# Performance work log

Measured on AMD Instinct MI355X. Metric: run time of the kernel, lower is better.

## Reference

```python
import jax, jax.numpy as jnp
import numpy as np

N, D, E = 50000, 128, 800000
NEG_SLOPE = 0.2


def setup_inputs() -> dict:
    key = jax.random.key(0)
    ks = jax.random.split(key, 16)
    src = jax.random.randint(ks[0], (E,), 0, N)
    dst = jax.random.randint(ks[1], (E,), 0, N)
    dst = jnp.where(src == dst, (dst + 1) % N, dst)  # no pre-existing self loops (PyG strips them)
    edge_index = jnp.stack([src, dst]).astype(jnp.int32)
    s = 1.0 / np.sqrt(D)  # glorot-ish scale
    return {
        'edge_index': edge_index,
        'embed': jax.random.normal(ks[2], (N, D), jnp.float32),
        'Wl1': jax.random.normal(ks[3], (D, D), jnp.float32) * s,
        'bl1': jnp.zeros((D,), jnp.float32),
        'Wr1': jax.random.normal(ks[4], (D, D), jnp.float32) * s,
        'br1': jnp.zeros((D,), jnp.float32),
        'att1': jax.random.normal(ks[5], (4, D // 4), jnp.float32) * s,
        'b1': jnp.zeros((D,), jnp.float32),
        'Wl2': jax.random.normal(ks[6], (D, D), jnp.float32) * s,
        'bl2': jnp.zeros((D,), jnp.float32),
        'Wr2': jax.random.normal(ks[7], (D, D), jnp.float32) * s,
        'br2': jnp.zeros((D,), jnp.float32),
        'att2': jax.random.normal(ks[8], (1, D), jnp.float32) * s,
        'b2': jnp.zeros((D,), jnp.float32),
    }


def gatv2(x, src, dst, Wl, bl, Wr, br, att, bias, heads, out_ch):
    n = x.shape[0]
    xl = (x @ Wl + bl).reshape(n, heads, out_ch)  # source-side messages
    xr = (x @ Wr + br).reshape(n, heads, out_ch)  # target-side
    e = jax.nn.leaky_relu(xl[src] + xr[dst], NEG_SLOPE)      # [E, H, C]
    score = jnp.einsum('ehc,hc->eh', e, att)                  # [E, H]
    # segment softmax over incoming edges of each target node
    smax = jax.ops.segment_max(score, dst, num_segments=n)
    ex = jnp.exp(score - smax[dst])
    denom = jax.ops.segment_sum(ex, dst, num_segments=n)
    alpha = ex / (denom[dst] + 1e-16)                         # [E, H]
    out = jax.ops.segment_sum(xl[src] * alpha[:, :, None], dst, num_segments=n)
    return out.reshape(n, heads * out_ch) + bias


def reference(edge_index, embed, Wl1, bl1, Wr1, br1, att1, b1,
              Wl2, bl2, Wr2, br2, att2, b2):
    loops = jnp.arange(N, dtype=edge_index.dtype)
    src = jnp.concatenate([edge_index[0], loops])  # add_self_loops=True (PyG default)
    dst = jnp.concatenate([edge_index[1], loops])
    x = gatv2(embed, src, dst, Wl1, bl1, Wr1, br1, att1, b1, 4, D // 4)
    x = jax.nn.relu(x)
    return gatv2(x, src, dst, Wl2, bl2, Wr2, br2, att2, b2, 1, D)
```

## Files before the change

kernel.cpp:

```cpp
#include <hip/hip_runtime.h>
#include <hip/hip_bf16.h>

#define NEG_SLOPE 0.2f
#define CAP 80
#define BNODES 256
#define BCAP 5120
#define CHUNK 4352

typedef unsigned short u16;
typedef short v8s __attribute__((ext_vector_type(8)));
typedef float v4f __attribute__((ext_vector_type(4)));

__device__ __forceinline__ u16 f32_to_bf16(float f) {
    unsigned u = __float_as_uint(f);
    u += 0x7fffu + ((u >> 16) & 1u);
    return (u16)(u >> 16);
}
__device__ __forceinline__ float4 bf16x4_to_f4(uint2 u) {
    float4 f;
    f.x = __uint_as_float(u.x << 16);
    f.y = __uint_as_float(u.x & 0xffff0000u);
    f.z = __uint_as_float(u.y << 16);
    f.w = __uint_as_float(u.y & 0xffff0000u);
    return f;
}

__global__ __launch_bounds__(256)
void prep(const float* __restrict__ Wa, const float* __restrict__ Wb,
          const float* __restrict__ Wc, const float* __restrict__ Wd,
          u16* __restrict__ dst, int* __restrict__ gcur, int nb)
{
    int g = blockIdx.x * 256 + threadIdx.x;
    if (g < nb) gcur[g] = 0;
    if (g >= 8192) return;
    int mat = g >> 11, rem = g & 2047;
    int f = rem >> 6, lane = rem & 63;
    int kt = f >> 3, nt = f & 7, q = lane >> 4, c = lane & 15;
    const float* W = (mat == 0) ? Wa : (mat == 1) ? Wb : (mat == 2) ? Wc : Wd;
    unsigned pk[4];
    #pragma unroll
    for (int jj = 0; jj < 4; ++jj) {
        float a = W[(kt * 32 + q * 8 + 2 * jj    ) * 128 + nt * 16 + c];
        float b = W[(kt * 32 + q * 8 + 2 * jj + 1) * 128 + nt * 16 + c];
        pk[jj] = (unsigned)f32_to_bf16(a) | ((unsigned)f32_to_bf16(b) << 16);
    }
    uint4 o; o.x = pk[0]; o.y = pk[1]; o.z = pk[2]; o.w = pk[3];
    *reinterpret_cast<uint4*>(dst + (size_t)mat * 16384 + ((size_t)f * 64 + lane) * 8) = o;
}

__global__ __launch_bounds__(256)
void bin_blocked(const int* __restrict__ esrc, const int* __restrict__ edst,
                 int e_in, int e_tot, int nb, int* __restrict__ gcur,
                 unsigned* __restrict__ barr)
{
    __shared__ unsigned ec[CHUNK];
    __shared__ int hist[BNODES], base[BNODES], offs[BNODES];
    const int t  = threadIdx.x;
    const int e0 = blockIdx.x * CHUNK;
    const int e1 = min(e_tot, e0 + CHUNK);

    for (int i = t; i < nb; i += 256) hist[i] = 0;
    __syncthreads();

    for (int e = e0 + t; e < e1; e += 256) {
        int s, d;
        if (e < e_in) { s = esrc[e]; d = edst[e]; } else { s = e - e_in; d = s; }
        int b = d >> 8, dl = d & 255;
        ec[e - e0] = (unsigned)s | ((unsigned)dl << 16) | ((unsigned)b << 24);
        atomicAdd(&hist[b], 1);
    }
    __syncthreads();

    for (int b = t; b < nb; b += 256) {
        offs[b] = 0;
        base[b] = hist[b] ? atomicAdd(&gcur[b], hist[b]) : 0;
    }
    __syncthreads();

    const int ce = e1 - e0;
    for (int i = t; i < ce; i += 256) {
        unsigned u = ec[i];
        int b = (int)(u >> 24);
        int pos = base[b] + atomicAdd(&offs[b], 1);
        if (pos < BCAP)
            barr[(size_t)b * BCAP + pos] = u & 0xffffffu;
    }
}

__global__ __launch_bounds__(256)
void bucket_build(const unsigned* __restrict__ barr, const int* __restrict__ gcur,
                  u16* __restrict__ slots, int* __restrict__ cnt)
{
    __shared__ u16 sl[BNODES * CAP];
    __shared__ int cnt_l[BNODES];
    const int b = blockIdx.x;
    const int t = threadIdx.x;
    cnt_l[t] = 0;
    __syncthreads();

    const int ce = min(gcur[b], BCAP);
    for (int i = t; i < ce; i += 256) {
        unsigned u = barr[(size_t)b * BCAP + i];
        int s  = (int)(u & 0xffffu);
        int dl = (int)(u >> 16);
        int pos = atomicAdd(&cnt_l[dl], 1);
        if (pos < CAP) sl[dl * CAP + pos] = (u16)s;
    }
    __syncthreads();

    const size_t base = (size_t)b * BNODES * CAP;
    uint4* dst = reinterpret_cast<uint4*>(slots + base);
    const uint4* src = reinterpret_cast<const uint4*>(sl);
    #pragma unroll
    for (int i = 0; i < (BNODES * CAP) / (8 * 256); ++i)
        dst[i * 256 + t] = src[i * 256 + t];
    cnt[b * BNODES + t] = min(cnt_l[t], CAP);
}

template<bool BF16_IN>
__global__ __launch_bounds__(256)
void gemm_mfma(const void* __restrict__ xin,
               const v8s* __restrict__ pwl, const v8s* __restrict__ pwr,
               const float* __restrict__ bl, const float* __restrict__ br,
               u16* __restrict__ outl, u16* __restrict__ outr, int n)
{
    __shared__ u16 xs[64 * 136];
    const int tid = threadIdx.x;
    const int node0 = blockIdx.x * 64;

    #pragma unroll
    for (int it = 0; it < 8; ++it) {
        int flat4 = it * 256 + tid;
        int row = flat4 >> 5;
        int col = (flat4 & 31) * 4;
        uint2 w = make_uint2(0u, 0u);
        if (node0 + row < n) {
            if (BF16_IN) {
                w = *reinterpret_cast<const uint2*>(
                        (const u16*)xin + (size_t)(node0 + row) * 128 + col);
            } else {
                float4 v = *reinterpret_cast<const float4*>(
                        (const float*)xin + (size_t)(node0 + row) * 128 + col);
                w.x = (unsigned)f32_to_bf16(v.x) | ((unsigned)f32_to_bf16(v.y) << 16);
                w.y = (unsigned)f32_to_bf16(v.z) | ((unsigned)f32_to_bf16(v.w) << 16);
            }
        }
        *reinterpret_cast<uint2*>(&xs[row * 136 + col]) = w;
    }
    __syncthreads();

    const int lane = tid & 63;
    const int wv   = tid >> 6;
    const int mat  = wv & 1;
    const int ch   = wv >> 1;
    const int q = lane >> 4, c = lane & 15;

    const v8s* __restrict__ pw     = mat ? pwr : pwl;
    const float* __restrict__ bias = mat ? br : bl;
    u16* __restrict__ outp         = mat ? outr : outl;

    v8s bfr[4][4];
    #pragma unroll
    for (int kt = 0; kt < 4; ++kt)
        #pragma unroll
        for (int nt = 0; nt < 4; ++nt)
            bfr[kt][nt] = pw[(kt * 8 + ch * 4 + nt) * 64 + lane];

    float bcol[4];
    #pragma unroll
    for (int nt = 0; nt < 4; ++nt) bcol[nt] = bias[ch * 64 + nt * 16 + c];

    #pragma unroll
    for (int mt = 0; mt < 4; ++mt) {
        const int arow = mt * 16 + c;
        v8s a[4];
        #pragma unroll
        for (int kt = 0; kt < 4; ++kt)
            a[kt] = *reinterpret_cast<const v8s*>(&xs[arow * 136 + kt * 32 + q * 8]);

        v4f acc0 = {0.f, 0.f, 0.f, 0.f};
        v4f acc1 = {0.f, 0.f, 0.f, 0.f};
        v4f acc2 = {0.f, 0.f, 0.f, 0.f};
        v4f acc3 = {0.f, 0.f, 0.f, 0.f};
        #pragma unroll
        for (int kt = 0; kt < 4; ++kt) {
            acc0 = __builtin_amdgcn_mfma_f32_16x16x32_bf16(a[kt], bfr[kt][0], acc0, 0, 0, 0);
            acc1 = __builtin_amdgcn_mfma_f32_16x16x32_bf16(a[kt], bfr[kt][1], acc1, 0, 0, 0);
            acc2 = __builtin_amdgcn_mfma_f32_16x16x32_bf16(a[kt], bfr[kt][2], acc2, 0, 0, 0);
            acc3 = __builtin_amdgcn_mfma_f32_16x16x32_bf16(a[kt], bfr[kt][3], acc3, 0, 0, 0);
        }

        #pragma unroll
        for (int r = 0; r < 4; ++r) {
            int node = node0 + mt * 16 + q * 4 + r;
            if (node < n) {
                size_t rb = (size_t)node * 128;
                outp[rb + ch * 64 +  0 + c] = f32_to_bf16(acc0[r] + bcol[0]);
                outp[rb + ch * 64 + 16 + c] = f32_to_bf16(acc1[r] + bcol[1]);
                outp[rb + ch * 64 + 32 + c] = f32_to_bf16(acc2[r] + bcol[2]);
                outp[rb + ch * 64 + 48 + c] = f32_to_bf16(acc3[r] + bcol[3]);
            }
        }
    }
}

template<int H>
__device__ __forceinline__ float edge_ex(float4 xlv, float4 xrv, float4 atv)
{
    float4 t = make_float4(xlv.x + xrv.x, xlv.y + xrv.y,
                           xlv.z + xrv.z, xlv.w + xrv.w);
    t.x = t.x > 0.f ? t.x : NEG_SLOPE * t.x;
    t.y = t.y > 0.f ? t.y : NEG_SLOPE * t.y;
    t.z = t.z > 0.f ? t.z : NEG_SLOPE * t.z;
    t.w = t.w > 0.f ? t.w : NEG_SLOPE * t.w;
    float p = t.x * atv.x + t.y * atv.y + t.z * atv.z + t.w * atv.w;
    p += __shfl_xor(p, 1);
    p += __shfl_xor(p, 2);
    p += __shfl_xor(p, 4);
    if (H == 1) {
        p += __shfl_xor(p, 8);
        p += __shfl_xor(p, 16);
    }
    return __expf(p);
}

template<int H, bool RELU_BF16_OUT>
__global__ __launch_bounds__(256)
void fused_attn(const u16* __restrict__ xl, const u16* __restrict__ xr,
                const float* __restrict__ att, const u16* __restrict__ slots,
                const int* __restrict__ cnt, const float* __restrict__ bias,
                void* __restrict__ outv, int n)
{
    int d = blockIdx.x * 8 + (threadIdx.x >> 5);
    if (d >= n) return;
    const int lane = threadIdx.x & 31;

    const float4 xrv = bf16x4_to_f4(
        *reinterpret_cast<const uint2*>(&xr[(size_t)d * 128 + lane * 4]));
    const float4 atv = *reinterpret_cast<const float4*>(&att[lane * 4]);

    const int start = d * CAP;
    const int end   = start + min(cnt[d], CAP);

    float4 acc0 = make_float4(0.f, 0.f, 0.f, 0.f);
    float4 acc1 = make_float4(0.f, 0.f, 0.f, 0.f);
    float4 acc2 = make_float4(0.f, 0.f, 0.f, 0.f);
    float4 acc3 = make_float4(0.f, 0.f, 0.f, 0.f);
    float  den0 = 0.f, den1 = 0.f, den2 = 0.f, den3 = 0.f;

    for (int base = start; base < end; base += 32) {
        const int cnt32 = min(32, end - base);
        int sidx = (base + lane < end) ? (int)slots[base + lane] : 0;
        int i = 0;
        for (; i + 4 <= cnt32; i += 4) {
            int s0 = __shfl(sidx, i, 32);
            int s1 = __shfl(sidx, i + 1, 32);
            int s2 = __shfl(sidx, i + 2, 32);
            int s3 = __shfl(sidx, i + 3, 32);
            float4 x0 = bf16x4_to_f4(*reinterpret_cast<const uint2*>(&xl[(size_t)s0 * 128 + lane * 4]));
            float4 x1 = bf16x4_to_f4(*reinterpret_cast<const uint2*>(&xl[(size_t)s1 * 128 + lane * 4]));
            float4 x2 = bf16x4_to_f4(*reinterpret_cast<const uint2*>(&xl[(size_t)s2 * 128 + lane * 4]));
            float4 x3 = bf16x4_to_f4(*reinterpret_cast<const uint2*>(&xl[(size_t)s3 * 128 + lane * 4]));
            float ex0 = edge_ex<H>(x0, xrv, atv);
            float ex1 = edge_ex<H>(x1, xrv, atv);
            float ex2 = edge_ex<H>(x2, xrv, atv);
            float ex3 = edge_ex<H>(x3, xrv, atv);
            den0 += ex0;
            acc0.x = fmaf(x0.x, ex0, acc0.x);
            acc0.y = fmaf(x0.y, ex0, acc0.y);
            acc0.z = fmaf(x0.z, ex0, acc0.z);
            acc0.w = fmaf(x0.w, ex0, acc0.w);
            den1 += ex1;
            acc1.x = fmaf(x1.x, ex1, acc1.x);
            acc1.y = fmaf(x1.y, ex1, acc1.y);
            acc1.z = fmaf(x1.z, ex1, acc1.z);
            acc1.w = fmaf(x1.w, ex1, acc1.w);
            den2 += ex2;
            acc2.x = fmaf(x2.x, ex2, acc2.x);
            acc2.y = fmaf(x2.y, ex2, acc2.y);
            acc2.z = fmaf(x2.z, ex2, acc2.z);
            acc2.w = fmaf(x2.w, ex2, acc2.w);
            den3 += ex3;
            acc3.x = fmaf(x3.x, ex3, acc3.x);
            acc3.y = fmaf(x3.y, ex3, acc3.y);
            acc3.z = fmaf(x3.z, ex3, acc3.z);
            acc3.w = fmaf(x3.w, ex3, acc3.w);
        }
        for (; i < cnt32; ++i) {
            int s0 = __shfl(sidx, i, 32);
            float4 x0 = bf16x4_to_f4(*reinterpret_cast<const uint2*>(&xl[(size_t)s0 * 128 + lane * 4]));
            float ex0 = edge_ex<H>(x0, xrv, atv);
            den0 += ex0;
            acc0.x = fmaf(x0.x, ex0, acc0.x);
            acc0.y = fmaf(x0.y, ex0, acc0.y);
            acc0.z = fmaf(x0.z, ex0, acc0.z);
            acc0.w = fmaf(x0.w, ex0, acc0.w);
        }
    }

    const float inv = 1.f / (den0 + den1 + den2 + den3 + 1e-16f);
    const float4 bv = *reinterpret_cast<const float4*>(&bias[lane * 4]);
    float4 r = make_float4((acc0.x + acc1.x + acc2.x + acc3.x) * inv + bv.x,
                           (acc0.y + acc1.y + acc2.y + acc3.y) * inv + bv.y,
                           (acc0.z + acc1.z + acc2.z + acc3.z) * inv + bv.z,
                           (acc0.w + acc1.w + acc2.w + acc3.w) * inv + bv.w);
    if (RELU_BF16_OUT) {
        r.x = fmaxf(r.x, 0.f); r.y = fmaxf(r.y, 0.f);
        r.z = fmaxf(r.z, 0.f); r.w = fmaxf(r.w, 0.f);
        uint2 o;
        o.x = (unsigned)f32_to_bf16(r.x) | ((unsigned)f32_to_bf16(r.y) << 16);
        o.y = (unsigned)f32_to_bf16(r.z) | ((unsigned)f32_to_bf16(r.w) << 16);
        *reinterpret_cast<uint2*>((u16*)outv + (size_t)d * 128 + lane * 4) = o;
    } else {
        *reinterpret_cast<float4*>((float*)outv + (size_t)d * 128 + lane * 4) = r;
    }
}


extern "C" void kernel_launch(void* const* d_in, const int* in_sizes, int n_in,
                              void* d_out, int out_size, void* d_ws, size_t ws_size,
                              hipStream_t stream)
{
    const int*   edge  = (const int*)d_in[0];
    const float* embed = (const float*)d_in[1];
    const float* Wl1   = (const float*)d_in[2];
    const float* bl1   = (const float*)d_in[3];
    const float* Wr1   = (const float*)d_in[4];
    const float* br1   = (const float*)d_in[5];
    const float* att1  = (const float*)d_in[6];
    const float* b1    = (const float*)d_in[7];
    const float* Wl2   = (const float*)d_in[8];
    const float* bl2   = (const float*)d_in[9];
    const float* Wr2   = (const float*)d_in[10];
    const float* br2   = (const float*)d_in[11];
    const float* att2  = (const float*)d_in[12];
    const float* b2    = (const float*)d_in[13];

    const int e_in  = in_sizes[0] / 2;
    const int n     = in_sizes[1] / 128;
    const int e_tot = e_in + n;
    const int NB    = (n + BNODES - 1) / BNODES;
    const int binb  = (e_tot + CHUNK - 1) / CHUNK;

    char* p = (char*)d_ws;
    u16* xl    = (u16*)p;  p += (size_t)n * 128 * 2;
    u16* xr    = (u16*)p;  p += (size_t)n * 128 * 2;
    u16* h1    = (u16*)p;  p += (size_t)n * 128 * 2;
    u16* wpack = (u16*)p;  p += (size_t)4 * 16384 * 2;
    int* gcur  = (int*)p;  p += (size_t)NB * 4;
    unsigned* barr = (unsigned*)p;  p += (size_t)NB * BCAP * 4;
    int* cnt   = (int*)p;  p += (size_t)NB * BNODES * 4;
    u16* slots = (u16*)p;
    float* out = (float*)d_out;

    const int* esrc = edge;
    const int* edst = edge + e_in;

    dim3 blk(256);
    const int gemm_blocks = (n + 63) / 64;
    const int node_blocks = (n + 7) / 8;

    prep<<<32, blk, 0, stream>>>(Wl1, Wr1, Wl2, Wr2, wpack, gcur, NB);
    bin_blocked<<<binb, blk, 0, stream>>>(esrc, edst, e_in, e_tot, NB, gcur, barr);
    bucket_build<<<NB, blk, 0, stream>>>(barr, gcur, slots, cnt);

    gemm_mfma<false><<<gemm_blocks, blk, 0, stream>>>(
        embed, (const v8s*)wpack, (const v8s*)(wpack + 16384),
        bl1, br1, xl, xr, n);
    fused_attn<4, true><<<node_blocks, blk, 0, stream>>>(
        xl, xr, att1, slots, cnt, b1, h1, n);

    gemm_mfma<true><<<gemm_blocks, blk, 0, stream>>>(
        h1, (const v8s*)(wpack + 32768), (const v8s*)(wpack + 49152),
        bl2, br2, xl, xr, n);
    fused_attn<1, false><<<node_blocks, blk, 0, stream>>>(
        xl, xr, att2, slots, cnt, b2, out, n);
}
```

Before: 245.2 us.

## Merge bucket build with layer-1 GEMM and add single-chunk fast path in attention

The bucket_build kernel and the first projection GEMM, which are independent, now run in one launch (phaseA) whose blocks dispatch by index, so the two overlap and one launch is saved. The fused attention kernel gains a fast path for nodes with at most 32 incoming edges: it loads the slot indices once and masks the tail of the last group of four, instead of running a scalar remainder loop. Leaky ReLU becomes fmaxf. The combined kernel allocates the larger shared-memory footprint (about 41 KB) for every block, including GEMM blocks that need much less, which may reduce GEMM occupancy.

```diff
diff --git a/kernel.cpp b/kernel.cpp
--- a/kernel.cpp
+++ b/kernel.cpp
@@ -87,13 +87,12 @@
     }
 }
 
-__global__ __launch_bounds__(256)
-void bucket_build(const unsigned* __restrict__ barr, const int* __restrict__ gcur,
-                  u16* __restrict__ slots, int* __restrict__ cnt)
-{
-    __shared__ u16 sl[BNODES * CAP];
-    __shared__ int cnt_l[BNODES];
-    const int b = blockIdx.x;
+__device__ __forceinline__ void bucket_body(char* smem, int b,
+    const unsigned* __restrict__ barr, const int* __restrict__ gcur,
+    u16* __restrict__ slots, int* __restrict__ cnt)
+{
+    u16* sl    = (u16*)smem;
+    int* cnt_l = (int*)(smem + BNODES * CAP * 2);
     const int t = threadIdx.x;
     cnt_l[t] = 0;
     __syncthreads();
@@ -118,15 +117,15 @@
 }
 
 template<bool BF16_IN>
-__global__ __launch_bounds__(256)
-void gemm_mfma(const void* __restrict__ xin,
-               const v8s* __restrict__ pwl, const v8s* __restrict__ pwr,
-               const float* __restrict__ bl, const float* __restrict__ br,
-               u16* __restrict__ outl, u16* __restrict__ outr, int n)
-{
-    __shared__ u16 xs[64 * 136];
+__device__ __forceinline__ void gemm_body(char* smem, int blk,
+    const void* __restrict__ xin,
+    const v8s* __restrict__ pwl, const v8s* __restrict__ pwr,
+    const float* __restrict__ bl, const float* __restrict__ br,
+    u16* __restrict__ outl, u16* __restrict__ outr, int n)
+{
+    u16* xs = (u16*)smem;
     const int tid = threadIdx.x;
-    const int node0 = blockIdx.x * 64;
+    const int node0 = blk * 64;
 
     #pragma unroll
     for (int it = 0; it < 8; ++it) {
@@ -204,15 +203,40 @@
     }
 }
 
+__global__ __launch_bounds__(256)
+void phaseA(const float* __restrict__ embed,
+            const v8s* __restrict__ pwl, const v8s* __restrict__ pwr,
+            const float* __restrict__ bl1, const float* __restrict__ br1,
+            u16* __restrict__ xl, u16* __restrict__ xr, int n, int gemm_blocks,
+            const unsigned* __restrict__ barr, const int* __restrict__ gcur,
+            u16* __restrict__ slots, int* __restrict__ cnt)
+{
+    __shared__ char smem[BNODES * CAP * 2 + BNODES * 4];
+    if ((int)blockIdx.x < gemm_blocks)
+        gemm_body<false>(smem, blockIdx.x, embed, pwl, pwr, bl1, br1, xl, xr, n);
+    else
+        bucket_body(smem, blockIdx.x - gemm_blocks, barr, gcur, slots, cnt);
+}
+
+__global__ __launch_bounds__(256)
+void gemm_mfma_bf16(const u16* __restrict__ xin,
+                    const v8s* __restrict__ pwl, const v8s* __restrict__ pwr,
+                    const float* __restrict__ bl, const float* __restrict__ br,
+                    u16* __restrict__ outl, u16* __restrict__ outr, int n)
+{
+    __shared__ char smem[64 * 136 * 2];
+    gemm_body<true>(smem, blockIdx.x, xin, pwl, pwr, bl, br, outl, outr, n);
+}
+
 template<int H>
 __device__ __forceinline__ float edge_ex(float4 xlv, float4 xrv, float4 atv)
 {
     float4 t = make_float4(xlv.x + xrv.x, xlv.y + xrv.y,
                            xlv.z + xrv.z, xlv.w + xrv.w);
-    t.x = t.x > 0.f ? t.x : NEG_SLOPE * t.x;
-    t.y = t.y > 0.f ? t.y : NEG_SLOPE * t.y;
-    t.z = t.z > 0.f ? t.z : NEG_SLOPE * t.z;
-    t.w = t.w > 0.f ? t.w : NEG_SLOPE * t.w;
+    t.x = fmaxf(t.x, NEG_SLOPE * t.x);
+    t.y = fmaxf(t.y, NEG_SLOPE * t.y);
+    t.z = fmaxf(t.z, NEG_SLOPE * t.z);
+    t.w = fmaxf(t.w, NEG_SLOPE * t.w);
     float p = t.x * atv.x + t.y * atv.y + t.z * atv.z + t.w * atv.w;
     p += __shfl_xor(p, 1);
     p += __shfl_xor(p, 2);
@@ -240,7 +264,7 @@
     const float4 atv = *reinterpret_cast<const float4*>(&att[lane * 4]);
 
     const int start = d * CAP;
-    const int end   = start + min(cnt[d], CAP);
+    const int k     = min(cnt[d], CAP);
 
     float4 acc0 = make_float4(0.f, 0.f, 0.f, 0.f);
     float4 acc1 = make_float4(0.f, 0.f, 0.f, 0.f);
@@ -248,15 +272,13 @@
     float4 acc3 = make_float4(0.f, 0.f, 0.f, 0.f);
     float  den0 = 0.f, den1 = 0.f, den2 = 0.f, den3 = 0.f;
 
-    for (int base = start; base < end; base += 32) {
-        const int cnt32 = min(32, end - base);
-        int sidx = (base + lane < end) ? (int)slots[base + lane] : 0;
-        int i = 0;
-        for (; i + 4 <= cnt32; i += 4) {
-            int s0 = __shfl(sidx, i, 32);
-            int s1 = __shfl(sidx, i + 1, 32);
-            int s2 = __shfl(sidx, i + 2, 32);
-            int s3 = __shfl(sidx, i + 3, 32);
+    if (__builtin_expect(k <= 32, 1)) {
+        int sidx = (lane < k) ? (int)slots[start + lane] : 0;
+        for (int i = 0; i < k; i += 4) {
+            int s0 = __shfl(sidx,  i,          32);
+            int s1 = __shfl(sidx, (i + 1) & 31, 32);
+            int s2 = __shfl(sidx, (i + 2) & 31, 32);
+            int s3 = __shfl(sidx, (i + 3) & 31, 32);
             float4 x0 = bf16x4_to_f4(*reinterpret_cast<const uint2*>(&xl[(size_t)s0 * 128 + lane * 4]));
             float4 x1 = bf16x4_to_f4(*reinterpret_cast<const uint2*>(&xl[(size_t)s1 * 128 + lane * 4]));
             float4 x2 = bf16x4_to_f4(*reinterpret_cast<const uint2*>(&xl[(size_t)s2 * 128 + lane * 4]));
@@ -265,6 +287,9 @@
             float ex1 = edge_ex<H>(x1, xrv, atv);
             float ex2 = edge_ex<H>(x2, xrv, atv);
             float ex3 = edge_ex<H>(x3, xrv, atv);
+            ex1 = (i + 1 < k) ? ex1 : 0.f;
+            ex2 = (i + 2 < k) ? ex2 : 0.f;
+            ex3 = (i + 3 < k) ? ex3 : 0.f;
             den0 += ex0;
             acc0.x = fmaf(x0.x, ex0, acc0.x);
             acc0.y = fmaf(x0.y, ex0, acc0.y);
@@ -286,15 +311,56 @@
             acc3.z = fmaf(x3.z, ex3, acc3.z);
             acc3.w = fmaf(x3.w, ex3, acc3.w);
         }
-        for (; i < cnt32; ++i) {
-            int s0 = __shfl(sidx, i, 32);
-            float4 x0 = bf16x4_to_f4(*reinterpret_cast<const uint2*>(&xl[(size_t)s0 * 128 + lane * 4]));
-            float ex0 = edge_ex<H>(x0, xrv, atv);
-            den0 += ex0;
-            acc0.x = fmaf(x0.x, ex0, acc0.x);
-            acc0.y = fmaf(x0.y, ex0, acc0.y);
-            acc0.z = fmaf(x0.z, ex0, acc0.z);
-            acc0.w = fmaf(x0.w, ex0, acc0.w);
+    } else {
+        const int end = start + k;
+        for (int base = start; base < end; base += 32) {
+            const int cnt32 = min(32, end - base);
+            int sidx = (base + lane < end) ? (int)slots[base + lane] : 0;
+            int i = 0;
+            for (; i + 4 <= cnt32; i += 4) {
+                int s0 = __shfl(sidx, i, 32);
+                int s1 = __shfl(sidx, i + 1, 32);
+                int s2 = __shfl(sidx, i + 2, 32);
+                int s3 = __shfl(sidx, i + 3, 32);
+                float4 x0 = bf16x4_to_f4(*reinterpret_cast<const uint2*>(&xl[(size_t)s0 * 128 + lane * 4]));
+                float4 x1 = bf16x4_to_f4(*reinterpret_cast<const uint2*>(&xl[(size_t)s1 * 128 + lane * 4]));
+                float4 x2 = bf16x4_to_f4(*reinterpret_cast<const uint2*>(&xl[(size_t)s2 * 128 + lane * 4]));
+                float4 x3 = bf16x4_to_f4(*reinterpret_cast<const uint2*>(&xl[(size_t)s3 * 128 + lane * 4]));
+                float ex0 = edge_ex<H>(x0, xrv, atv);
+                float ex1 = edge_ex<H>(x1, xrv, atv);
+                float ex2 = edge_ex<H>(x2, xrv, atv);
+                float ex3 = edge_ex<H>(x3, xrv, atv);
+                den0 += ex0;
+                acc0.x = fmaf(x0.x, ex0, acc0.x);
+                acc0.y = fmaf(x0.y, ex0, acc0.y);
+                acc0.z = fmaf(x0.z, ex0, acc0.z);
+                acc0.w = fmaf(x0.w, ex0, acc0.w);
+                den1 += ex1;
+                acc1.x = fmaf(x1.x, ex1, acc1.x);
+                acc1.y = fmaf(x1.y, ex1, acc1.y);
+                acc1.z = fmaf(x1.z, ex1, acc1.z);
+                acc1.w = fmaf(x1.w, ex1, acc1.w);
+                den2 += ex2;
+                acc2.x = fmaf(x2.x, ex2, acc2.x);
+                acc2.y = fmaf(x2.y, ex2, acc2.y);
+                acc2.z = fmaf(x2.z, ex2, acc2.z);
+                acc2.w = fmaf(x2.w, ex2, acc2.w);
+                den3 += ex3;
+                acc3.x = fmaf(x3.x, ex3, acc3.x);
+                acc3.y = fmaf(x3.y, ex3, acc3.y);
+                acc3.z = fmaf(x3.z, ex3, acc3.z);
+                acc3.w = fmaf(x3.w, ex3, acc3.w);
+            }
+            for (; i < cnt32; ++i) {
+                int s0 = __shfl(sidx, i, 32);
+                float4 x0 = bf16x4_to_f4(*reinterpret_cast<const uint2*>(&xl[(size_t)s0 * 128 + lane * 4]));
+                float ex0 = edge_ex<H>(x0, xrv, atv);
+                den0 += ex0;
+                acc0.x = fmaf(x0.x, ex0, acc0.x);
+                acc0.y = fmaf(x0.y, ex0, acc0.y);
+                acc0.z = fmaf(x0.z, ex0, acc0.z);
+                acc0.w = fmaf(x0.w, ex0, acc0.w);
+            }
         }
     }
 
@@ -362,15 +428,13 @@
 
     prep<<<32, blk, 0, stream>>>(Wl1, Wr1, Wl2, Wr2, wpack, gcur, NB);
     bin_blocked<<<binb, blk, 0, stream>>>(esrc, edst, e_in, e_tot, NB, gcur, barr);
-    bucket_build<<<NB, blk, 0, stream>>>(barr, gcur, slots, cnt);
-
-    gemm_mfma<false><<<gemm_blocks, blk, 0, stream>>>(
+    phaseA<<<gemm_blocks + NB, blk, 0, stream>>>(
         embed, (const v8s*)wpack, (const v8s*)(wpack + 16384),
-        bl1, br1, xl, xr, n);
+        bl1, br1, xl, xr, n, gemm_blocks, barr, gcur, slots, cnt);
+
     fused_attn<4, true><<<node_blocks, blk, 0, stream>>>(
         xl, xr, att1, slots, cnt, b1, h1, n);
-
-    gemm_mfma<true><<<gemm_blocks, blk, 0, stream>>>(
+    gemm_mfma_bf16<<<gemm_blocks, blk, 0, stream>>>(
         h1, (const v8s*)(wpack + 32768), (const v8s*)(wpack + 49152),
         bl2, br2, xl, xr, n);
     fused_attn<1, false><<<node_blocks, blk, 0, stream>>>(
```

Measured after the change: 236.9 us. 3.4% less time.
